# Kernel tuning notes

Measured on AMD Instinct MI355X. Metric: run time of the kernel, lower is better.

Reference implementation:

```python
import jax, jax.numpy as jnp
import numpy as np

B, T, C, L = 256, 1024, 128, 64
BLANK = C - 1          # tf.compat.v1.nn.ctc_loss uses num_classes-1 as blank
EPS = 1e-7             # keras.backend.epsilon()
NEG = -1e30            # log-space 'zero'
S = 2 * L + 1          # extended label length (blanks interleaved)


def setup_inputs() -> dict:
    key = jax.random.key(0)
    k1, k2 = jax.random.split(key)
    # y_pred are softmax probabilities (the layer takes log(y_pred + eps))
    y_pred = jax.nn.softmax(jax.random.normal(k1, (B, T, C), dtype=jnp.float32), axis=-1)
    # labels in [0, C-2]; blank (C-1) never appears in targets
    y_true = jax.random.randint(k2, (B, L), 0, C - 1, dtype=jnp.int32)
    return {"y_true": y_true, "y_pred": y_pred}


def _ctc_loss(y_true, y_pred):
    logp = jnp.log(y_pred + EPS)                                   # [B,T,C]
    # extended label sequence: blank, l1, blank, l2, ..., blank -> [B,S]
    ext = jnp.full((B, S), BLANK, dtype=jnp.int32).at[:, 1::2].set(y_true)
    # gather per-extended-symbol log-probs: lp_ext[b,t,s] = logp[b,t,ext[b,s]]
    lp_ext = jnp.take_along_axis(logp[:, :, None, :], ext[:, None, :, None], axis=-1)[..., 0]  # [B,T,S]
    lp_ext = jnp.transpose(lp_ext, (1, 0, 2))                      # [T,B,S] time-major for scan
    # skip transition allowed where ext[s] != blank and ext[s] != ext[s-2]
    can_skip = jnp.concatenate(
        [jnp.zeros((B, 2), dtype=bool), (ext[:, 2:] != BLANK) & (ext[:, 2:] != ext[:, :-2])],
        axis=1)                                                    # [B,S]

    def shift(a, n):
        return jnp.concatenate([jnp.full((B, n), NEG, a.dtype), a[:, : S - n]], axis=1)

    # alpha init at t=0: only s=0 (blank) and s=1 (first label) reachable
    alpha0 = (jnp.full((B, S), NEG)
              .at[:, 0].set(lp_ext[0, :, 0])
              .at[:, 1].set(lp_ext[0, :, 1]))

    def step(alpha, lp_t):
        s1 = shift(alpha, 1)
        s2 = jnp.where(can_skip, shift(alpha, 2), NEG)
        m = jnp.maximum(alpha, jnp.maximum(s1, s2))                # stable log-sum-exp of 3 terms
        new = m + jnp.log(jnp.exp(alpha - m) + jnp.exp(s1 - m) + jnp.exp(s2 - m)) + lp_t
        return new, None

    alphaT, _ = jax.lax.scan(step, alpha0, lp_ext[1:])
    log_lik = jnp.logaddexp(alphaT[:, -1], alphaT[:, -2])          # end in last blank or last label
    return (-log_lik)[:, None]                                     # [B,1], matches expand_dims(..., 1)


def reference(y_true, y_pred):
    return _ctc_loss(y_true, y_pred)
```

## Files before the change

### kernel.cpp

```cpp
#include <hip/hip_runtime.h>


#define B_     256
#define T_     1024
#define C_     128
#define L_     64
#define BLANK_ 127
#define EPS_   1e-7f
#define LN2_   0.69314718055994530942f
#define ROWS   32
#define LDSF   (ROWS * C_)

__device__ __forceinline__ float flog2(float x) { return __builtin_amdgcn_logf(x); }

template <int CTRL>
__device__ __forceinline__ int dpp_i(int x) {
    return __builtin_amdgcn_update_dpp(x, x, CTRL, 0xF, 0xF, false);
}
__device__ __forceinline__ float ror1_f(float x) {
    return __int_as_float(dpp_i<0x13C>(__float_as_int(x)));
}
__device__ __forceinline__ int ror1_i(int x) { return dpp_i<0x13C>(x); }

__device__ __forceinline__ float fldexp(float x, int n) {
#if __has_builtin(__builtin_amdgcn_ldexpf)
    return __builtin_amdgcn_ldexpf(x, n);
#else
    return ldexpf(x, n);
#endif
}
__device__ __forceinline__ int fexp_of(float x) {
#if __has_builtin(__builtin_amdgcn_frexp_expf)
    return __builtin_amdgcn_frexp_expf(x);
#else
    const int bx = (__float_as_int(x) >> 23) & 0xFF;
    return (x > 0.0f) ? (bx - 126) : 0;
#endif
}

typedef const __attribute__((address_space(1))) void gas_void;
typedef __attribute__((address_space(3))) void las_void;
__device__ __forceinline__ void g2l16(const float* g, float* l) {
    __builtin_amdgcn_global_load_lds((gas_void*)g, (las_void*)l, 16, 0, 0);
}
__device__ __forceinline__ void g2l4(const float* g, float* l) {
    __builtin_amdgcn_global_load_lds((gas_void*)g, (las_void*)l, 4, 0, 0);
}

#define LSTEP(pL, pB)                                                         \
    {                                                                         \
        const float pBe = (pB) + EPS_;                                        \
        const float pLe = (pL) + EPS_;                                        \
        const int   ep  = ror1_i(e);                                          \
        const float mpE = ror1_f(aE);                                         \
        const float mpO = ror1_f(aO);                                         \
        const bool dead = (fmaxf(aE, aO) == 0.0f);                            \
        e = dead ? ep : e;                                                    \
        const int   d   = ep - e;                                             \
        float prevE = fldexp(mpE, d);                                         \
        const float prevO = fldexp(mpO, d);                                   \
        prevE = isL0 ? fldexp(a0, e0 - e) : prevE;                            \
        const float sk = can_skip ? prevO : 0.0f;                             \
        const float nE = (aE + aO) * pBe;                                     \
        const float nO = (aO + prevE + sk) * pLe;                             \
        a0 *= pBe;                                                            \
        aE = nE; aO = nO;                                                     \
    }

#define RENORM4                                                               \
    {                                                                         \
        const int x = fexp_of(fmaxf(aE, aO));                                 \
        aE = fldexp(aE, -x); aO = fldexp(aO, -x); e += x;                     \
        const int x0 = fexp_of(a0);                                           \
        a0 = fldexp(a0, -x0); e0 += x0;                                       \
    }

#define STAGE_CHUNK(k, LOFF)                                                  \
    {                                                                         \
        const float* src = base + (size_t)(1 + 32 * (k)) * C_;                \
        const int nKB = ((k) == 31) ? 15 : 16;                                \
        for (int j = 0; j < nKB; ++j)                                         \
            g2l16(src + j * 256 + lane * 4, sm + (LOFF) + j * 256);           \
        if ((k) == 31) {                                                      \
            const float* s2 = src + 15 * 256;                                 \
            g2l4(s2 + lane,      sm + (LOFF) + 15 * 256);                     \
            g2l4(s2 + 64 + lane, sm + (LOFF) + 15 * 256 + 64);                \
        }                                                                     \
    }

#define BURST(LOFF, RL, RB, NR)                                               \
    {                                                                         \
        _Pragma("unroll")                                                     \
        for (int j = 0; j < (NR); ++j) {                                      \
            RL[j] = sm[(LOFF) + j * C_ + lab];                                \
            RB[j] = sm[(LOFF) + j * C_ + BLANK_];                             \
        }                                                                     \
    }

#define CHUNK_COMPUTE(RL, RB, NS)                                             \
    {                                                                         \
        _Pragma("unroll")                                                     \
        for (int k = 0; k < (NS); ++k) {                                      \
            LSTEP(RL[k], RB[k])                                               \
            if ((k & 3) == 3) RENORM4                                         \
        }                                                                     \
    }

#define VMWAIT asm volatile("s_waitcnt vmcnt(0)" ::: "memory")

__global__ __launch_bounds__(64, 1)
void ctc_fwd(const int* __restrict__ yt, const float* __restrict__ yp,
             float* __restrict__ out) {
    __shared__ float sm[3 * LDSF];

    const int b    = blockIdx.x;
    const int lane = threadIdx.x;
    const int lab  = yt[b * L_ + lane];
    const int labp = __shfl_up(lab, 1);
    const bool can_skip = (lane > 0) && (lab != labp);
    const bool isL0     = (lane == 0);

    const float* __restrict__ base = yp + (size_t)b * T_ * C_;

    STAGE_CHUNK(0, 0)
    STAGE_CHUNK(1, LDSF)

    float a0 = base[BLANK_] + EPS_;
    float aO = isL0 ? (base[lab] + EPS_) : 0.0f;
    float aE = 0.0f;
    int   e  = 0, e0 = 0;

    VMWAIT;

    float rLA[32], rBA[32], rLB[32], rBB[32];
    BURST(0, rLA, rBA, 32)

#pragma unroll 1
    for (int c = 0; c < 30; c += 2) {
        {
            const int lo_s = ((c + 2) % 3) * LDSF;
            const int lo_b = ((c + 1) % 3) * LDSF;
            STAGE_CHUNK(c + 2, lo_s)
            BURST(lo_b, rLB, rBB, 32)
            CHUNK_COMPUTE(rLA, rBA, 32)
            VMWAIT;
        }
        {
            const int lo_s = ((c + 3) % 3) * LDSF;
            const int lo_b = ((c + 2) % 3) * LDSF;
            STAGE_CHUNK(c + 3, lo_s)
            BURST(lo_b, rLA, rBA, 32)
            CHUNK_COMPUTE(rLB, rBB, 32)
            VMWAIT;
        }
    }

    {
        const int lo_b = (31 % 3) * LDSF;
        BURST(lo_b, rLB, rBB, 31)
        CHUNK_COMPUTE(rLA, rBA, 32)
    }

    CHUNK_COMPUTE(rLB, rBB, 31)

    if (lane == 63) {
        const float s = aE + aO;
        out[b] = -(flog2(s) + (float)e) * LN2_;
    }
}

extern "C" void kernel_launch(void* const* d_in, const int* in_sizes, int n_in,
                              void* d_out, int out_size, void* d_ws, size_t ws_size,
                              hipStream_t stream) {
    const int*   y_true = (const int*)d_in[0];
    const float* y_pred = (const float*)d_in[1];
    float*       out    = (float*)d_out;
    ctc_fwd<<<B_, 64, 0, stream>>>(y_true, y_pred, out);
}
```

Measured before the change: 206.9 us.

## Use wave-uniform scale exponent with premultiplied probabilities and sparser renormalization

Drops the per-lane exponent bookkeeping, where each lane carried its own scale and shifted neighbour values by the exponent difference. All lanes now share one exponent, found every 16 steps by a DPP max-reduction across the wave. Each probability is premultiplied by 128 to slow underflow between renormalizations, and the final result subtracts the accumulated 7*1023 offset. This removes several ldexp and select ops from the serial per-step recurrence. The risk is underflow for lanes far below the wave maximum, which a shared scale cannot rescue.

```diff
diff --git a/kernel.cpp b/kernel.cpp
--- a/kernel.cpp
+++ b/kernel.cpp
@@ -10,6 +10,8 @@
 #define LN2_   0.69314718055994530942f
 #define ROWS   32
 #define LDSF   (ROWS * C_)
+#define PRE_   128.0f
+#define EPSP_  (EPS_ * PRE_)
 
 __device__ __forceinline__ float flog2(float x) { return __builtin_amdgcn_logf(x); }
 
@@ -20,7 +22,10 @@
 __device__ __forceinline__ float ror1_f(float x) {
     return __int_as_float(dpp_i<0x13C>(__float_as_int(x)));
 }
-__device__ __forceinline__ int ror1_i(int x) { return dpp_i<0x13C>(x); }
+template <int CTRL>
+__device__ __forceinline__ float maxlvl(float m) {
+    return fmaxf(m, __int_as_float(dpp_i<CTRL>(__float_as_int(m))));
+}
 
 __device__ __forceinline__ float fldexp(float x, int n) {
 #if __has_builtin(__builtin_amdgcn_ldexpf)
@@ -49,30 +54,31 @@
 
 #define LSTEP(pL, pB)                                                         \
     {                                                                         \
-        const float pBe = (pB) + EPS_;                                        \
-        const float pLe = (pL) + EPS_;                                        \
-        const int   ep  = ror1_i(e);                                          \
+        const float pBe = __builtin_fmaf((pB), PRE_, EPSP_);                  \
+        const float pLe = __builtin_fmaf((pL), PRE_, EPSP_);                  \
         const float mpE = ror1_f(aE);                                         \
         const float mpO = ror1_f(aO);                                         \
-        const bool dead = (fmaxf(aE, aO) == 0.0f);                            \
-        e = dead ? ep : e;                                                    \
-        const int   d   = ep - e;                                             \
-        float prevE = fldexp(mpE, d);                                         \
-        const float prevO = fldexp(mpO, d);                                   \
-        prevE = isL0 ? fldexp(a0, e0 - e) : prevE;                            \
-        const float sk = can_skip ? prevO : 0.0f;                             \
+        const float prevE = isL0 ? a0 : mpE;                                  \
+        const float sk    = can_skip ? mpO : 0.0f;                            \
         const float nE = (aE + aO) * pBe;                                     \
         const float nO = (aO + prevE + sk) * pLe;                             \
         a0 *= pBe;                                                            \
         aE = nE; aO = nO;                                                     \
     }
 
-#define RENORM4                                                               \
+#define RENORM16                                                              \
     {                                                                         \
-        const int x = fexp_of(fmaxf(aE, aO));                                 \
-        aE = fldexp(aE, -x); aO = fldexp(aO, -x); e += x;                     \
-        const int x0 = fexp_of(a0);                                           \
-        a0 = fldexp(a0, -x0); e0 += x0;                                       \
+        float m = fmaxf(fmaxf(aE, aO), a0);                                   \
+        m = maxlvl<0x111>(m);                                                 \
+        m = maxlvl<0x112>(m);                                                 \
+        m = maxlvl<0x114>(m);                                                 \
+        m = maxlvl<0x118>(m);                                                 \
+        m = maxlvl<0x142>(m);                                                 \
+        m = maxlvl<0x143>(m);                                                 \
+        const int x = fexp_of(__int_as_float(                                 \
+            __builtin_amdgcn_readlane(__float_as_int(m), 63)));               \
+        aE = fldexp(aE, -x); aO = fldexp(aO, -x); a0 = fldexp(a0, -x);        \
+        e += x;                                                               \
     }
 
 #define STAGE_CHUNK(k, LOFF)                                                  \
@@ -102,7 +108,7 @@
         _Pragma("unroll")                                                     \
         for (int k = 0; k < (NS); ++k) {                                      \
             LSTEP(RL[k], RB[k])                                               \
-            if ((k & 3) == 3) RENORM4                                         \
+            if ((k & 15) == 15) RENORM16                                      \
         }                                                                     \
     }
 
@@ -128,7 +134,7 @@
     float a0 = base[BLANK_] + EPS_;
     float aO = isL0 ? (base[lab] + EPS_) : 0.0f;
     float aE = 0.0f;
-    int   e  = 0, e0 = 0;
+    int   e  = 0;
 
     VMWAIT;
 
@@ -165,7 +171,7 @@
 
     if (lane == 63) {
         const float s = aE + aO;
-        out[b] = -(flog2(s) + (float)e) * LN2_;
+        out[b] = -(flog2(s) + (float)(e - 7161)) * LN2_;
     }
 }
 
```

New measurement: 196.7 us. -4.9%, faster.

## Replace 32-row register bursts with a rolling 4-deep LDS prefetch pipeline

Applied to the files above, without the earlier changes.

Each chunk no longer loads 32 rows of label and blank probabilities into large register arrays up front. The kernel now keeps a rolling 4-entry register buffer, loading the LDS value for step t+4 while computing step t, and loops over groups of 4 with unroll 1. It also marks the staging loop unroll 1. This cuts register pressure and code size, but the loop overhead and the short prefetch distance could expose LDS latency on the serial recurrence.

```diff
diff --git a/kernel.cpp b/kernel.cpp
--- a/kernel.cpp
+++ b/kernel.cpp
@@ -79,30 +79,13 @@
     {                                                                         \
         const float* src = base + (size_t)(1 + 32 * (k)) * C_;                \
         const int nKB = ((k) == 31) ? 15 : 16;                                \
+        _Pragma("unroll 1")                                                   \
         for (int j = 0; j < nKB; ++j)                                         \
             g2l16(src + j * 256 + lane * 4, sm + (LOFF) + j * 256);           \
         if ((k) == 31) {                                                      \
             const float* s2 = src + 15 * 256;                                 \
             g2l4(s2 + lane,      sm + (LOFF) + 15 * 256);                     \
             g2l4(s2 + 64 + lane, sm + (LOFF) + 15 * 256 + 64);                \
-        }                                                                     \
-    }
-
-#define BURST(LOFF, RL, RB, NR)                                               \
-    {                                                                         \
-        _Pragma("unroll")                                                     \
-        for (int j = 0; j < (NR); ++j) {                                      \
-            RL[j] = sm[(LOFF) + j * C_ + lab];                                \
-            RB[j] = sm[(LOFF) + j * C_ + BLANK_];                             \
-        }                                                                     \
-    }
-
-#define CHUNK_COMPUTE(RL, RB, NS)                                             \
-    {                                                                         \
-        _Pragma("unroll")                                                     \
-        for (int k = 0; k < (NS); ++k) {                                      \
-            LSTEP(RL[k], RB[k])                                               \
-            if ((k & 3) == 3) RENORM4                                         \
         }                                                                     \
     }
 
@@ -132,36 +115,72 @@
 
     VMWAIT;
 
-    float rLA[32], rBA[32], rLB[32], rBB[32];
-    BURST(0, rLA, rBA, 32)
+    float rL[4], rB[4];
+#pragma unroll
+    for (int j = 0; j < 4; ++j) {
+        rL[j] = sm[j * C_ + lab];
+        rB[j] = sm[j * C_ + BLANK_];
+    }
 
 #pragma unroll 1
-    for (int c = 0; c < 30; c += 2) {
-        {
-            const int lo_s = ((c + 2) % 3) * LDSF;
-            const int lo_b = ((c + 1) % 3) * LDSF;
-            STAGE_CHUNK(c + 2, lo_s)
-            BURST(lo_b, rLB, rBB, 32)
-            CHUNK_COMPUTE(rLA, rBA, 32)
-            VMWAIT;
+    for (int c = 0; c < 31; ++c) {
+        const int bc = (c % 3) * LDSF;
+        const int bn = ((c + 1) % 3) * LDSF;
+        if (c <= 29)
+            STAGE_CHUNK(c + 2, ((c + 2) % 3) * LDSF)
+        const float* pf = &sm[bc + 4 * C_];
+#pragma unroll 1
+        for (int g = 0; g < 7; ++g) {
+#pragma unroll
+            for (int j = 0; j < 4; ++j) {
+                const float pL = rL[j];
+                const float pB = rB[j];
+                rL[j] = pf[lab];
+                rB[j] = pf[BLANK_];
+                pf += C_;
+                LSTEP(pL, pB)
+            }
+            RENORM4
         }
         {
-            const int lo_s = ((c + 3) % 3) * LDSF;
-            const int lo_b = ((c + 2) % 3) * LDSF;
-            STAGE_CHUNK(c + 3, lo_s)
-            BURST(lo_b, rLA, rBA, 32)
-            CHUNK_COMPUTE(rLB, rBB, 32)
-            VMWAIT;
+            const float* pn = &sm[bn];
+#pragma unroll
+            for (int j = 0; j < 4; ++j) {
+                const float pL = rL[j];
+                const float pB = rB[j];
+                rL[j] = pn[lab];
+                rB[j] = pn[BLANK_];
+                pn += C_;
+                LSTEP(pL, pB)
+            }
+            RENORM4
         }
+        VMWAIT;
     }
 
     {
-        const int lo_b = (31 % 3) * LDSF;
-        BURST(lo_b, rLB, rBB, 31)
-        CHUNK_COMPUTE(rLA, rBA, 32)
+        const int bc = (31 % 3) * LDSF;
+        const float* pf = &sm[bc + 4 * C_];
+#pragma unroll 1
+        for (int g = 0; g < 7; ++g) {
+#pragma unroll
+            for (int j = 0; j < 4; ++j) {
+                const float pL = rL[j];
+                const float pB = rB[j];
+                rL[j] = pf[lab];
+                rB[j] = pf[BLANK_];
+                pf += C_;
+                LSTEP(pL, pB)
+            }
+            RENORM4
+        }
+#pragma unroll
+        for (int j = 0; j < 3; ++j) {
+            const float pL = rL[j];
+            const float pB = rB[j];
+            LSTEP(pL, pB)
+        }
     }
-
-    CHUNK_COMPUTE(rLB, rBB, 31)
 
     if (lane == 63) {
         const float s = aE + aO;
```

Measured after the change: 224.4 us. 8.5% more time.

## Remap lanes so each lane holds blank-before and label, drop separate a0 track

Applied to the files above, without the earlier changes.

Reassigns the per-lane state so each lane holds the blank preceding its label plus the label, with an extra trailing-blank accumulator that shares the lane exponent. Only one cross-lane DPP rotate per step is then needed, and the separate lane-0 exponent tracking goes away. After the first few chunks, once every lane's exponent is live, a cheaper step variant runs that reuses an exponent difference computed only at each renormalisation and uses an FMA for the skip term. This shortens the serial per-timestep dependency chain, but it relies on the exponent difference between neighbouring lanes staying fixed between renormalisations.

```diff
diff --git a/kernel.cpp b/kernel.cpp
--- a/kernel.cpp
+++ b/kernel.cpp
@@ -47,40 +47,76 @@
     __builtin_amdgcn_global_load_lds((gas_void*)g, (las_void*)l, 4, 0, 0);
 }
 
-#define LSTEP(pL, pB)                                                         \
+#define ALSTEP(pL, pB)                                                        \
     {                                                                         \
         const float pBe = (pB) + EPS_;                                        \
         const float pLe = (pL) + EPS_;                                        \
         const int   ep  = ror1_i(e);                                          \
-        const float mpE = ror1_f(aE);                                         \
         const float mpO = ror1_f(aO);                                         \
         const bool dead = (fmaxf(aE, aO) == 0.0f);                            \
         e = dead ? ep : e;                                                    \
-        const int   d   = ep - e;                                             \
-        float prevE = fldexp(mpE, d);                                         \
-        const float prevO = fldexp(mpO, d);                                   \
-        prevE = isL0 ? fldexp(a0, e0 - e) : prevE;                            \
+        const int   dd  = ep - e;                                             \
+        float prevO = fldexp(mpO, dd);                                        \
+        prevO = isL0 ? 0.0f : prevO;                                          \
         const float sk = can_skip ? prevO : 0.0f;                             \
-        const float nE = (aE + aO) * pBe;                                     \
-        const float nO = (aO + prevE + sk) * pLe;                             \
-        a0 *= pBe;                                                            \
+        const float nE = (aE + prevO) * pBe;                                  \
+        const float nO = (aO + aE + sk) * pLe;                                \
+        aZ = (aZ + aO) * pBe;                                                 \
         aE = nE; aO = nO;                                                     \
     }
 
 #define RENORM4                                                               \
     {                                                                         \
         const int x = fexp_of(fmaxf(aE, aO));                                 \
-        aE = fldexp(aE, -x); aO = fldexp(aO, -x); e += x;                     \
-        const int x0 = fexp_of(a0);                                           \
-        a0 = fldexp(a0, -x0); e0 += x0;                                       \
+        aE = fldexp(aE, -x); aO = fldexp(aO, -x); aZ = fldexp(aZ, -x);        \
+        e += x;                                                               \
+    }
+
+#define DCALC                                                                 \
+    {                                                                         \
+        const int ep = ror1_i(e);                                             \
+        d = isL0 ? (-16384) : (ep - e);                                       \
+    }
+
+#define RENORM4B { RENORM4 DCALC }
+
+#define BLSTEP(pL, pB)                                                        \
+    {                                                                         \
+        const float pBe = (pB) + EPS_;                                        \
+        const float pLe = (pL) + EPS_;                                        \
+        const float prevO = fldexp(ror1_f(aO), d);                            \
+        const float nE = (aE + prevO) * pBe;                                  \
+        const float nO = __builtin_fmaf(skf, prevO, aO + aE) * pLe;           \
+        aZ = (aZ + aO) * pBe;                                                 \
+        aE = nE; aO = nO;                                                     \
+    }
+
+#define ACHUNK(RL, RB)                                                        \
+    {                                                                         \
+        _Pragma("unroll")                                                     \
+        for (int k = 0; k < 32; ++k) {                                        \
+            ALSTEP(RL[k], RB[k])                                              \
+            if ((k & 3) == 3) RENORM4                                         \
+        }                                                                     \
+    }
+
+#define BCHUNK32(RL, RB)                                                      \
+    {                                                                         \
+        _Pragma("unroll")                                                     \
+        for (int k = 0; k < 32; ++k) {                                        \
+            BLSTEP(RL[k], RB[k])                                              \
+            if ((k & 3) == 3) RENORM4B                                        \
+        }                                                                     \
     }
 
 #define STAGE_CHUNK(k, LOFF)                                                  \
     {                                                                         \
         const float* src = base + (size_t)(1 + 32 * (k)) * C_;                \
         const int nKB = ((k) == 31) ? 15 : 16;                                \
-        for (int j = 0; j < nKB; ++j)                                         \
-            g2l16(src + j * 256 + lane * 4, sm + (LOFF) + j * 256);           \
+        _Pragma("unroll")                                                     \
+        for (int j = 0; j < 16; ++j)                                          \
+            if (j < nKB)                                                      \
+                g2l16(src + j * 256 + lane * 4, sm + (LOFF) + j * 256);       \
         if ((k) == 31) {                                                      \
             const float* s2 = src + 15 * 256;                                 \
             g2l4(s2 + lane,      sm + (LOFF) + 15 * 256);                     \
@@ -94,15 +130,6 @@
         for (int j = 0; j < (NR); ++j) {                                      \
             RL[j] = sm[(LOFF) + j * C_ + lab];                                \
             RB[j] = sm[(LOFF) + j * C_ + BLANK_];                             \
-        }                                                                     \
-    }
-
-#define CHUNK_COMPUTE(RL, RB, NS)                                             \
-    {                                                                         \
-        _Pragma("unroll")                                                     \
-        for (int k = 0; k < (NS); ++k) {                                      \
-            LSTEP(RL[k], RB[k])                                               \
-            if ((k & 3) == 3) RENORM4                                         \
         }                                                                     \
     }
 
@@ -119,52 +146,72 @@
     const int labp = __shfl_up(lab, 1);
     const bool can_skip = (lane > 0) && (lab != labp);
     const bool isL0     = (lane == 0);
+    const float skf     = can_skip ? 1.0f : 0.0f;
 
     const float* __restrict__ base = yp + (size_t)b * T_ * C_;
 
     STAGE_CHUNK(0, 0)
     STAGE_CHUNK(1, LDSF)
 
-    float a0 = base[BLANK_] + EPS_;
-    float aO = isL0 ? (base[lab] + EPS_) : 0.0f;
-    float aE = 0.0f;
-    int   e  = 0, e0 = 0;
-
-    VMWAIT;
-
-    float rLA[32], rBA[32], rLB[32], rBB[32];
-    BURST(0, rLA, rBA, 32)
+    float aE = isL0 ? (base[BLANK_] + EPS_) : 0.0f;
+    float aO = isL0 ? (base[lab]    + EPS_) : 0.0f;
+    float aZ = 0.0f;
+    int   e  = 0, d = 0;
+
+    VMWAIT;
+
+    float rl0[32], rb0[32], rl1[32], rb1[32];
+    BURST(0, rl0, rb0, 32)
+
+    STAGE_CHUNK(2, 2 * LDSF)
+    BURST(LDSF, rl1, rb1, 32)
+    ACHUNK(rl0, rb0)
+    VMWAIT;
+
+    STAGE_CHUNK(3, 0)
+    BURST(2 * LDSF, rl0, rb0, 32)
+    ACHUNK(rl1, rb1)
+    VMWAIT;
+
+    STAGE_CHUNK(4, LDSF)
+    BURST(0, rl1, rb1, 32)
+    ACHUNK(rl0, rb0)
+    VMWAIT;
+
+    STAGE_CHUNK(5, 2 * LDSF)
+    BURST(LDSF, rl0, rb0, 32)
+    ACHUNK(rl1, rb1)
+    VMWAIT;
+
+    DCALC
 
 #pragma unroll 1
-    for (int c = 0; c < 30; c += 2) {
+    for (int c = 4; c <= 28; c += 2) {
         {
-            const int lo_s = ((c + 2) % 3) * LDSF;
-            const int lo_b = ((c + 1) % 3) * LDSF;
-            STAGE_CHUNK(c + 2, lo_s)
-            BURST(lo_b, rLB, rBB, 32)
-            CHUNK_COMPUTE(rLA, rBA, 32)
+            STAGE_CHUNK(c + 2, ((c + 2) % 3) * LDSF)
+            BURST(((c + 1) % 3) * LDSF, rl1, rb1, 32)
+            BCHUNK32(rl0, rb0)
             VMWAIT;
         }
         {
-            const int lo_s = ((c + 3) % 3) * LDSF;
-            const int lo_b = ((c + 2) % 3) * LDSF;
-            STAGE_CHUNK(c + 3, lo_s)
-            BURST(lo_b, rLA, rBA, 32)
-            CHUNK_COMPUTE(rLB, rBB, 32)
+            STAGE_CHUNK(c + 3, ((c + 3) % 3) * LDSF)
+            BURST(((c + 2) % 3) * LDSF, rl0, rb0, 32)
+            BCHUNK32(rl1, rb1)
             VMWAIT;
         }
     }
 
-    {
-        const int lo_b = (31 % 3) * LDSF;
-        BURST(lo_b, rLB, rBB, 31)
-        CHUNK_COMPUTE(rLA, rBA, 32)
-    }
-
-    CHUNK_COMPUTE(rLB, rBB, 31)
+    BURST((31 % 3) * LDSF, rl1, rb1, 31)
+    BCHUNK32(rl0, rb0)
+
+#pragma unroll
+    for (int k = 0; k < 31; ++k) {
+        BLSTEP(rl1[k], rb1[k])
+        if ((k & 3) == 3) RENORM4B
+    }
 
     if (lane == 63) {
-        const float s = aE + aO;
+        const float s = aO + aZ;
         out[b] = -(flog2(s) + (float)e) * LN2_;
     }
 }
```

After: 198.1 us. 4.2% less time.
